# Kernel tuning notes

Hardware: AMD Instinct MI355X
Metric: run time of the kernel (lower is better)

## Reference

```python
import jax, jax.numpy as jnp
import numpy as np

N = 100000   # nodes
E = 600000   # edges
D = 128      # in_dim == out_dim
ED = 6       # edge_dim
LN_EPS = 1e-5


def setup_inputs() -> dict:
    key = jax.random.key(0)
    ks = jax.random.split(key, 12)
    s = 1.0 / np.sqrt(D)
    se = 1.0 / np.sqrt(ED)
    return {
        "x": jax.random.normal(ks[0], (N, D), dtype=jnp.float32),
        "edge_index": jax.random.randint(ks[1], (2, E), 0, N, dtype=jnp.int64),
        "edge_attr": jax.random.normal(ks[2], (E, ED), dtype=jnp.float32),
        "batch": jnp.zeros((N,), dtype=jnp.int64),
        "W_e": jax.random.uniform(ks[3], (ED, D), jnp.float32, -se, se),
        "b_e": jax.random.uniform(ks[4], (D,), jnp.float32, -se, se),
        "eps": jnp.zeros((), dtype=jnp.float32),  # GINE train_eps init 0
        "W1": jax.random.uniform(ks[5], (D, D), jnp.float32, -s, s),
        "b1": jax.random.uniform(ks[6], (D,), jnp.float32, -s, s),
        "W2": jax.random.uniform(ks[7], (D, D), jnp.float32, -s, s),
        "b2": jax.random.uniform(ks[8], (D,), jnp.float32, -s, s),
        "gamma": jnp.ones((D,), dtype=jnp.float32),
        "beta": jnp.zeros((D,), dtype=jnp.float32),
    }


def reference(x, edge_index, edge_attr, batch, W_e, b_e, eps, W1, b1, W2, b2, gamma, beta):
    src, dst = edge_index[0], edge_index[1]
    # edge embedding: Linear(edge_dim -> in_dim)
    edge_emb = edge_attr @ W_e + b_e                      # [E, D]
    # GINEConv message: ReLU(x_j + edge_emb), scatter-add to target nodes
    msg = jax.nn.relu(x[src] + edge_emb)                  # [E, D]
    agg = jax.ops.segment_sum(msg, dst, num_segments=N)   # [N, D]
    h = (1.0 + eps) * x + agg                             # [N, D]
    # GINE nn: Linear -> ReLU -> Linear
    h = jax.nn.relu(h @ W1 + b1) @ W2 + b2                # [N, D]
    # LayerNorm over feature dim
    mu = jnp.mean(h, axis=-1, keepdims=True)
    var = jnp.var(h, axis=-1, keepdims=True)
    h = (h - mu) * jax.lax.rsqrt(var + LN_EPS) * gamma + beta
    # activation=True -> ReLU; dropout identity in eval mode
    return jax.nn.relu(h)
```

## Files before the change

### kernel.cpp

```cpp
#include <hip/hip_runtime.h>
#include <stdint.h>

#define NN 100000
#define EE 600000
#define DD 128

typedef _Float16 half8 __attribute__((ext_vector_type(8)));
typedef _Float16 h2 __attribute__((ext_vector_type(2)));
typedef float f32x4 __attribute__((ext_vector_type(4)));

static __device__ __forceinline__ uint32_t pack2(float a, float b) {
    h2 h; h.x = (_Float16)a; h.y = (_Float16)b;
    return __builtin_bit_cast(uint32_t, h);
}
static __device__ __forceinline__ h2 cvt22(float2 f) {
    h2 r; r.x = (_Float16)f.x; r.y = (_Float16)f.y; return r;
}
static __device__ __forceinline__ h2 bc_lo(h2 v) { h2 r; r.x = v.x; r.y = v.x; return r; }
static __device__ __forceinline__ h2 bc_hi(h2 v) { h2 r; r.x = v.y; r.y = v.y; return r; }

static __device__ __forceinline__ uint32_t edge_msg2(uint32_t rY, uint32_t rZ, uint32_t rW,
                                                     uint32_t xv, uint32_t bb,
                                                     uint32_t w0, uint32_t w1, uint32_t w2,
                                                     uint32_t w3, uint32_t w4, uint32_t w5)
{
    uint32_t m;
    asm("v_pk_fma_f16 %0, %1, %2, %3 op_sel:[0,0,0] op_sel_hi:[0,1,1]"
        : "=v"(m) : "v"(rY), "v"(w0), "v"(bb));
    asm("v_pk_fma_f16 %0, %1, %2, %0 op_sel:[1,0,0] op_sel_hi:[1,1,1]" : "+v"(m) : "v"(rY), "v"(w1));
    asm("v_pk_fma_f16 %0, %1, %2, %0 op_sel:[0,0,0] op_sel_hi:[0,1,1]" : "+v"(m) : "v"(rZ), "v"(w2));
    asm("v_pk_fma_f16 %0, %1, %2, %0 op_sel:[1,0,0] op_sel_hi:[1,1,1]" : "+v"(m) : "v"(rZ), "v"(w3));
    asm("v_pk_fma_f16 %0, %1, %2, %0 op_sel:[0,0,0] op_sel_hi:[0,1,1]" : "+v"(m) : "v"(rW), "v"(w4));
    asm("v_pk_fma_f16 %0, %1, %2, %0 op_sel:[1,0,0] op_sel_hi:[1,1,1]" : "+v"(m) : "v"(rW), "v"(w5));
    asm("v_pk_add_f16 %0, %0, %1" : "+v"(m) : "v"(xv));
    asm("v_pk_max_f16 %0, %0, 0" : "+v"(m));
    return m;
}

#define NB_HIST ((EE + 255) / 256)
#define NB_CONV (NN * DD / 4 / 256)
template<bool CONV>
__global__ __launch_bounds__(256)
void setup_kernel(const int* __restrict__ ei, const float* __restrict__ x,
                  const float* __restrict__ W1, const float* __restrict__ W2,
                  int* __restrict__ counts, uint32_t* __restrict__ xh,
                  _Float16* __restrict__ w1h, _Float16* __restrict__ w2h)
{
    const int nbc = CONV ? NB_CONV : 0;
    const int b = blockIdx.x, tid = threadIdx.x;
    if (b < NB_HIST) {
        int e = b * 256 + tid;
        if (e < EE) atomicAdd(&counts[ei[EE + e]], 1);
    } else if (CONV && b < NB_HIST + nbc) {
        int i = (b - NB_HIST) * 256 + tid;
        float4 v = ((const float4*)x)[i];
        uint2 o; o.x = pack2(v.x, v.y); o.y = pack2(v.z, v.w);
        ((uint2*)xh)[i] = o;
    } else {
        int t = (b - NB_HIST - nbc) * 256 + tid;
        if (t < 2 * DD * DD) {
            int which = t >> 14;
            int idx = t & (DD * DD - 1);
            int k = idx >> 7, d = idx & 127;
            float wv = (which ? W2 : W1)[k * DD + d];
            int kt = k >> 5, kr = k & 31;
            int grp = kr >> 3, j = kr & 7;
            int nt = d >> 4, cc = d & 15;
            int off = ((kt * 8 + nt) * 64 + grp * 16 + cc) * 8 + j;
            (which ? w2h : w1h)[off] = (_Float16)wv;
        }
    }
}

__global__ __launch_bounds__(256)
void scan_blocks(const int* __restrict__ counts, int* __restrict__ startv,
                 int* __restrict__ bsum)
{
    const int t = threadIdx.x;
    const int idx = blockIdx.x * 1024 + t * 4;
    int4 v = {0, 0, 0, 0};
    if (idx < NN) v = *(const int4*)(counts + idx);
    int s1 = v.x + v.y, s2 = s1 + v.z, s3 = s2 + v.w;
    const int lane = t & 63;
    int q = s3;
#pragma unroll
    for (int off = 1; off < 64; off <<= 1) {
        int u = __shfl_up(q, off, 64);
        if (lane >= off) q += u;
    }
    __shared__ int wsum[4];
    if (lane == 63) wsum[t >> 6] = q;
    __syncthreads();
    const int w = t >> 6;
    int pre = 0;
    if (w > 0) pre += wsum[0];
    if (w > 1) pre += wsum[1];
    if (w > 2) pre += wsum[2];
    const int excl = (q - s3) + pre;
    if (idx < NN) {
        int4 o = {excl, excl + v.x, excl + s1, excl + s2};
        *(int4*)(startv + idx) = o;
    }
    __syncthreads();
    if (t == 0) bsum[blockIdx.x] = wsum[0] + wsum[1] + wsum[2] + wsum[3];
}

__global__ __launch_bounds__(128)
void scan_top(const int* __restrict__ bsum, int* __restrict__ boff)
{
    __shared__ int sm[128];
    const int t = threadIdx.x;
    const int NB = (NN + 1023) / 1024;
    int v = (t < NB) ? bsum[t] : 0;
    sm[t] = v;
    __syncthreads();
#pragma unroll
    for (int off = 1; off < 128; off <<= 1) {
        int u = (t >= off) ? sm[t - off] : 0;
        __syncthreads();
        sm[t] += u;
        __syncthreads();
    }
    boff[t] = sm[t] - v;
}

__global__ __launch_bounds__(256)
void scatter_rec(const int* __restrict__ ei, const float* __restrict__ ea,
                 const int* __restrict__ start, const int* __restrict__ boff,
                 int* __restrict__ cursor, float* __restrict__ rec)
{
    int e = blockIdx.x * 256 + threadIdx.x;
    if (e >= EE) return;
    int dst = ei[EE + e];
    int src = ei[e];
    int pos = start[dst] + boff[dst >> 10] + atomicAdd(&cursor[dst], 1);
    const float2* eap = (const float2*)(ea + e * 6);
    float2 e01 = eap[0];
    float2 e23 = eap[1];
    float2 e45 = eap[2];
    float4 r;
    r.x = __int_as_float(src << 6);
    r.y = __uint_as_float(pack2(e01.x, e01.y));
    r.z = __uint_as_float(pack2(e23.x, e23.y));
    r.w = __uint_as_float(pack2(e45.x, e45.y));
    *(float4*)(rec + (size_t)pos * 4) = r;
}

#define NWAVE 8192
__global__ __launch_bounds__(256)
void agg_stream(const uint32_t* __restrict__ xh,
                const float4* __restrict__ rec, const float* __restrict__ We,
                const float* __restrict__ be, const int* __restrict__ start,
                const int* __restrict__ boff, const float* __restrict__ epsp,
                uint32_t* __restrict__ h0h)
{
    const int w = blockIdx.x * 4 + (threadIdx.x >> 6);
    const int lane = threadIdx.x & 63;
    const int d0 = lane * 2;
    const uint32_t w0u = __builtin_bit_cast(uint32_t, cvt22(*(const float2*)(We + 0 * DD + d0)));
    const uint32_t w1u = __builtin_bit_cast(uint32_t, cvt22(*(const float2*)(We + 1 * DD + d0)));
    const uint32_t w2u = __builtin_bit_cast(uint32_t, cvt22(*(const float2*)(We + 2 * DD + d0)));
    const uint32_t w3u = __builtin_bit_cast(uint32_t, cvt22(*(const float2*)(We + 3 * DD + d0)));
    const uint32_t w4u = __builtin_bit_cast(uint32_t, cvt22(*(const float2*)(We + 4 * DD + d0)));
    const uint32_t w5u = __builtin_bit_cast(uint32_t, cvt22(*(const float2*)(We + 5 * DD + d0)));
    const uint32_t bbu = __builtin_bit_cast(uint32_t, cvt22(*(const float2*)(be + d0)));
    const float sc = 1.0f + epsp[0];
    const int n0 = (int)(((long long)w * NN) >> 13);
    const int n1 = (int)(((long long)(w + 1) * NN) >> 13);
    const int span = n1 - n0;

    int gs = 0;
    {
        int nidx = n0 + lane;
        if (lane <= span) {
            gs = (nidx < NN) ? (start[nidx] + boff[nidx >> 10]) : EE;
        }
    }
    const int ebase = __shfl(gs, 0, 64);
    const int eend  = __shfl(gs, span, 64);

    int n = n0;
    int nstop = __shfl(gs, 1, 64);
    h2 xnh = __builtin_bit_cast(h2, xh[((uint32_t)n0 << 6) + lane]);
    float ax = 0.f, ay = 0.f;

#define STEP(K, MK)                                                              \
    {                                                                            \
        const int ek = e + K;                                                    \
        if (ek < eend) {                                                         \
            while (ek >= nstop) {                                                \
                h0h[(size_t)n * 64 + lane] =                                     \
                    pack2(fmaf(sc, (float)xnh.x, ax), fmaf(sc, (float)xnh.y, ay)); \
                ax = 0.f; ay = 0.f; ++n;                                         \
                xnh = __builtin_bit_cast(h2, xh[((uint32_t)n << 6) + lane]);     \
                nstop = __shfl(gs, n - n0 + 1, 64);                              \
            }                                                                    \
            h2 mh = __builtin_bit_cast(h2, MK);                                  \
            ax += (float)mh.x; ay += (float)mh.y;                                \
        }                                                                        \
    }

    for (int e = ebase; e < eend; e += 8) {
        const int last = eend - 1;
        int idx[8];
        float4 r[8];
        uint32_t xv[8], m[8];
#pragma unroll
        for (int k = 0; k < 8; ++k) {
            int ik = e + k;
            idx[k] = ik < eend ? ik : last;
        }
#pragma unroll
        for (int k = 0; k < 8; ++k) r[k] = rec[idx[k]];
#pragma unroll
        for (int k = 0; k < 8; ++k)
            xv[k] = xh[(uint32_t)__float_as_int(r[k].x) + lane];
#pragma unroll
        for (int k = 0; k < 8; ++k)
            m[k] = edge_msg2(__float_as_uint(r[k].y), __float_as_uint(r[k].z),
                             __float_as_uint(r[k].w), xv[k], bbu,
                             w0u, w1u, w2u, w3u, w4u, w5u);
        STEP(0, m[0])
        STEP(1, m[1])
        STEP(2, m[2])
        STEP(3, m[3])
        STEP(4, m[4])
        STEP(5, m[5])
        STEP(6, m[6])
        STEP(7, m[7])
    }
#undef STEP

    while (n < n1) {
        h0h[(size_t)n * 64 + lane] = pack2(fmaf(sc, (float)xnh.x, ax), fmaf(sc, (float)xnh.y, ay));
        ax = 0.f; ay = 0.f; ++n;
        if (n < n1) xnh = __builtin_bit_cast(h2, xh[((uint32_t)n << 6) + lane]);
    }
}

__global__ __launch_bounds__(256)
void agg_pk(const float* __restrict__ x, const float* __restrict__ rec,
            const float* __restrict__ We, const float* __restrict__ be,
            const int* __restrict__ start, const int* __restrict__ boff,
            const int* __restrict__ counts, const float* __restrict__ epsp,
            uint32_t* __restrict__ h0h)
{
    const int w = blockIdx.x * 4 + (threadIdx.x >> 6);
    const int lane = threadIdx.x & 63;
    const int d0 = lane * 2;
    const h2 w0h = cvt22(*(const float2*)(We + 0 * DD + d0));
    const h2 w1h = cvt22(*(const float2*)(We + 1 * DD + d0));
    const h2 w2h = cvt22(*(const float2*)(We + 2 * DD + d0));
    const h2 w3h = cvt22(*(const float2*)(We + 3 * DD + d0));
    const h2 w4h = cvt22(*(const float2*)(We + 4 * DD + d0));
    const h2 w5h = cvt22(*(const float2*)(We + 5 * DD + d0));
    const h2 bbh = cvt22(*(const float2*)(be + d0));
    h2 zero2; zero2.x = (_Float16)0.f; zero2.y = (_Float16)0.f;
    const float sc = 1.0f + epsp[0];
    const int n0 = (int)(((long long)w * NN) >> 13);
    const int n1 = (int)(((long long)(w + 1) * NN) >> 13);

    for (int n = n0; n < n1; ++n) {
        const int begin = start[n] + boff[n >> 10];
        const int cnt = counts[n];
        const float4* rp = (const float4*)rec + begin;
        float ax = 0.f, ay = 0.f;
        for (int i = 0; i < cnt; ++i) {
            float4 r = rp[i];
            int s64 = __float_as_int(r.x);
            h2 c01 = __builtin_bit_cast(h2, r.y);
            h2 c23 = __builtin_bit_cast(h2, r.z);
            h2 c45 = __builtin_bit_cast(h2, r.w);
            h2 emb = bbh;
            emb = bc_lo(c01) * w0h + emb;
            emb = bc_hi(c01) * w1h + emb;
            emb = bc_lo(c23) * w2h + emb;
            emb = bc_hi(c23) * w3h + emb;
            emb = bc_lo(c45) * w4h + emb;
            emb = bc_hi(c45) * w5h + emb;
            h2 m = emb + cvt22(*(const float2*)(x + (size_t)s64 * 2 + d0));
            m = __builtin_elementwise_max(m, zero2);
            ax += (float)m.x;
            ay += (float)m.y;
        }
        float2 xn = *(const float2*)(x + (size_t)n * DD + d0);
        h0h[(size_t)n * 64 + lane] = pack2(fmaf(sc, xn.x, ax), fmaf(sc, xn.y, ay));
    }
}

__global__ __launch_bounds__(256)
void prep_w(const float* __restrict__ W1, const float* __restrict__ W2,
            _Float16* __restrict__ w1h, _Float16* __restrict__ w2h)
{
    int t = blockIdx.x * 256 + threadIdx.x;
    if (t >= 2 * DD * DD) return;
    int which = t >> 14;
    int idx = t & (DD * DD - 1);
    int k = idx >> 7, d = idx & 127;
    float wv = (which ? W2 : W1)[k * DD + d];
    int kt = k >> 5, kr = k & 31;
    int grp = kr >> 3, j = kr & 7;
    int nt = d >> 4, cc = d & 15;
    int off = ((kt * 8 + nt) * 64 + grp * 16 + cc) * 8 + j;
    (which ? w2h : w1h)[off] = (_Float16)wv;
}

__global__ __launch_bounds__(256)
void edge_kernel(const float* __restrict__ x, const int* __restrict__ ei,
                 const float* __restrict__ ea, const float* __restrict__ We,
                 const float* __restrict__ be, float* agg)
{
    int tid = blockIdx.x * 256 + threadIdx.x;
    int d0 = (tid & 31) * 4;
    float4 w0 = *(const float4*)(We + 0 * DD + d0);
    float4 w1 = *(const float4*)(We + 1 * DD + d0);
    float4 w2 = *(const float4*)(We + 2 * DD + d0);
    float4 w3 = *(const float4*)(We + 3 * DD + d0);
    float4 w4 = *(const float4*)(We + 4 * DD + d0);
    float4 w5 = *(const float4*)(We + 5 * DD + d0);
    float4 bb = *(const float4*)(be + d0);
    int estride = (gridDim.x * 256) >> 5;
    for (int e = tid >> 5; e < EE; e += estride) {
        int src = ei[e];
        int dst = ei[EE + e];
        const float2* eap = (const float2*)(ea + e * 6);
        float2 e01 = eap[0];
        float2 e23 = eap[1];
        float2 e45 = eap[2];
        float4 xj = *(const float4*)(x + (size_t)src * DD + d0);
        float mx = xj.x + bb.x + e01.x*w0.x + e01.y*w1.x + e23.x*w2.x + e23.y*w3.x + e45.x*w4.x + e45.y*w5.x;
        float my = xj.y + bb.y + e01.x*w0.y + e01.y*w1.y + e23.x*w2.y + e23.y*w3.y + e45.x*w4.y + e45.y*w5.y;
        float mz = xj.z + bb.z + e01.x*w0.z + e01.y*w1.z + e23.x*w2.z + e23.y*w3.z + e45.x*w4.z + e45.y*w5.z;
        float mw = xj.w + bb.w + e01.x*w0.w + e01.y*w1.w + e23.x*w2.w + e23.y*w3.w + e45.x*w4.w + e45.y*w5.w;
        float* ap = agg + (size_t)dst * DD + d0;
        atomicAdd(ap + 0, fmaxf(mx, 0.f));
        atomicAdd(ap + 1, fmaxf(my, 0.f));
        atomicAdd(ap + 2, fmaxf(mz, 0.f));
        atomicAdd(ap + 3, fmaxf(mw, 0.f));
    }
}

__global__ __launch_bounds__(256)
void node_f16(const uint32_t* __restrict__ h0h,
              const _Float16* __restrict__ w1h, const _Float16* __restrict__ w2h,
              const float* __restrict__ b1, const float* __restrict__ b2,
              const float* __restrict__ gamma, const float* __restrict__ beta,
              float* __restrict__ out)
{
    __shared__ _Float16 h1buf[4][16 * 128];
    const int wv = threadIdx.x >> 6;
    const int l  = threadIdx.x & 63;
    const int lm = l & 15;
    const int lg = l >> 4;
    const int rbase = blockIdx.x * 128 + wv * 32;

    float gam[8], bet[8];
#pragma unroll
    for (int nt = 0; nt < 8; ++nt) {
        gam[nt] = gamma[nt * 16 + lm];
        bet[nt] = beta[nt * 16 + lm];
    }

    for (int t = 0; t < 2; ++t) {
        const int r0 = rbase + t * 16;
        int arow = r0 + lm;
        if (arow >= NN) arow = NN - 1;

        half8 a1[4];
#pragma unroll
        for (int kt = 0; kt < 4; ++kt) {
            const int kb = kt * 32 + lg * 8;
            a1[kt] = *(const half8*)((const _Float16*)h0h + (size_t)arow * DD + kb);
        }

        f32x4 acc[8];
#pragma unroll
        for (int nt = 0; nt < 8; ++nt) { acc[nt][0]=0.f; acc[nt][1]=0.f; acc[nt][2]=0.f; acc[nt][3]=0.f; }
#pragma unroll
        for (int kt = 0; kt < 4; ++kt) {
#pragma unroll
            for (int nt = 0; nt < 8; ++nt) {
                half8 bh = *(const half8*)(w1h + ((size_t)((kt * 8 + nt) * 64 + l)) * 8);
                acc[nt] = __builtin_amdgcn_mfma_f32_16x16x32_f16(a1[kt], bh, acc[nt], 0, 0, 0);
            }
        }

        _Float16* hb = h1buf[wv];
#pragma unroll
        for (int nt = 0; nt < 8; ++nt) {
            const int col = nt * 16 + lm;
            const float bias = b1[col];
#pragma unroll
            for (int q = 0; q < 4; ++q) {
                const int row = lg * 4 + q;
                float v1 = fmaxf(acc[nt][q] + bias, 0.f);
                hb[row * 128 + (col ^ ((row & 7) << 4))] = (_Float16)v1;
            }
        }

        half8 a2[4];
        {
            const int sw = (lm & 7) << 4;
            const _Float16* rowp = hb + lm * 128;
#pragma unroll
            for (int kt = 0; kt < 4; ++kt) {
                const int kb = kt * 32 + lg * 8;
                a2[kt] = *(const half8*)(rowp + (kb ^ sw));
            }
        }

        f32x4 acc2[8];
#pragma unroll
        for (int nt = 0; nt < 8; ++nt) { acc2[nt][0]=0.f; acc2[nt][1]=0.f; acc2[nt][2]=0.f; acc2[nt][3]=0.f; }
#pragma unroll
        for (int kt = 0; kt < 4; ++kt) {
#pragma unroll
            for (int nt = 0; nt < 8; ++nt) {
                half8 bh = *(const half8*)(w2h + ((size_t)((kt * 8 + nt) * 64 + l)) * 8);
                acc2[nt] = __builtin_amdgcn_mfma_f32_16x16x32_f16(a2[kt], bh, acc2[nt], 0, 0, 0);
            }
        }

        float vv[8][4];
        float sums[4] = {0,0,0,0}, sqs[4] = {0,0,0,0};
#pragma unroll
        for (int nt = 0; nt < 8; ++nt) {
            const int col = nt * 16 + lm;
            const float bias = b2[col];
#pragma unroll
            for (int q = 0; q < 4; ++q) {
                float v2 = acc2[nt][q] + bias;
                vv[nt][q] = v2;
                sums[q] += v2;
                sqs[q]  += v2 * v2;
            }
        }
#pragma unroll
        for (int m = 1; m < 16; m <<= 1) {
#pragma unroll
            for (int q = 0; q < 4; ++q) {
                sums[q] += __shfl_xor(sums[q], m, 64);
                sqs[q]  += __shfl_xor(sqs[q],  m, 64);
            }
        }
#pragma unroll
        for (int q = 0; q < 4; ++q) {
            const int grow = r0 + lg * 4 + q;
            if (grow < NN) {
                const float mu  = sums[q] * (1.f / 128.f);
                const float var = sqs[q] * (1.f / 128.f) - mu * mu;
                const float rs  = rsqrtf(var + 1e-5f);
#pragma unroll
                for (int nt = 0; nt < 8; ++nt) {
                    out[(size_t)grow * DD + nt * 16 + lm] =
                        fmaxf((vv[nt][q] - mu) * rs * gam[nt] + bet[nt], 0.f);
                }
            }
        }
    }
}

__global__ __launch_bounds__(256)
void node2c(const float* __restrict__ aggp, const float* __restrict__ xp,
            const _Float16* __restrict__ w1h, const _Float16* __restrict__ w2h,
            const float* __restrict__ b1, const float* __restrict__ b2,
            const float* __restrict__ gamma, const float* __restrict__ beta,
            const float* __restrict__ epsp, float* __restrict__ out)
{
    __shared__ _Float16 h1buf[4][16 * 128];
    const int wv = threadIdx.x >> 6;
    const int l  = threadIdx.x & 63;
    const int lm = l & 15;
    const int lg = l >> 4;
    const int rbase = blockIdx.x * 128 + wv * 32;

    float gam[8], bet[8];
#pragma unroll
    for (int nt = 0; nt < 8; ++nt) {
        gam[nt] = gamma[nt * 16 + lm];
        bet[nt] = beta[nt * 16 + lm];
    }

    for (int t = 0; t < 2; ++t) {
        const int r0 = rbase + t * 16;
        int arow = r0 + lm;
        if (arow >= NN) arow = NN - 1;

        half8 a1[4];
#pragma unroll
        for (int kt = 0; kt < 4; ++kt) {
            const int kb = kt * 32 + lg * 8;
            const float4* hp = (const float4*)(aggp + (size_t)arow * DD + kb);
            float4 p0 = hp[0], p1 = hp[1];
            const float scale = 1.0f + epsp[0];
            const float4* xr = (const float4*)(xp + (size_t)arow * DD + kb);
            float4 x0 = xr[0], x1 = xr[1];
            float v[8] = { x0.x*scale+p0.x, x0.y*scale+p0.y, x0.z*scale+p0.z, x0.w*scale+p0.w,
                           x1.x*scale+p1.x, x1.y*scale+p1.y, x1.z*scale+p1.z, x1.w*scale+p1.w };
#pragma unroll
            for (int j = 0; j < 8; ++j) a1[kt][j] = (_Float16)v[j];
        }

        f32x4 acc[8];
#pragma unroll
        for (int nt = 0; nt < 8; ++nt) { acc[nt][0]=0.f; acc[nt][1]=0.f; acc[nt][2]=0.f; acc[nt][3]=0.f; }
#pragma unroll
        for (int kt = 0; kt < 4; ++kt) {
#pragma unroll
            for (int nt = 0; nt < 8; ++nt) {
                half8 bh = *(const half8*)(w1h + ((size_t)((kt * 8 + nt) * 64 + l)) * 8);
                acc[nt] = __builtin_amdgcn_mfma_f32_16x16x32_f16(a1[kt], bh, acc[nt], 0, 0, 0);
            }
        }

        _Float16* hb = h1buf[wv];
#pragma unroll
        for (int nt = 0; nt < 8; ++nt) {
            const int col = nt * 16 + lm;
            const float bias = b1[col];
#pragma unroll
            for (int q = 0; q < 4; ++q) {
                const int row = lg * 4 + q;
                float v1 = fmaxf(acc[nt][q] + bias, 0.f);
                hb[row * 128 + (col ^ ((row & 7) << 4))] = (_Float16)v1;
            }
        }

        half8 a2[4];
        {
            const int sw = (lm & 7) << 4;
            const _Float16* rowp = hb + lm * 128;
#pragma unroll
            for (int kt = 0; kt < 4; ++kt) {
                const int kb = kt * 32 + lg * 8;
                a2[kt] = *(const half8*)(rowp + (kb ^ sw));
            }
        }

        f32x4 acc2[8];
#pragma unroll
        for (int nt = 0; nt < 8; ++nt) { acc2[nt][0]=0.f; acc2[nt][1]=0.f; acc2[nt][2]=0.f; acc2[nt][3]=0.f; }
#pragma unroll
        for (int kt = 0; kt < 4; ++kt) {
#pragma unroll
            for (int nt = 0; nt < 8; ++nt) {
                half8 bh = *(const half8*)(w2h + ((size_t)((kt * 8 + nt) * 64 + l)) * 8);
                acc2[nt] = __builtin_amdgcn_mfma_f32_16x16x32_f16(a2[kt], bh, acc2[nt], 0, 0, 0);
            }
        }

        float vv[8][4];
        float sums[4] = {0,0,0,0}, sqs[4] = {0,0,0,0};
#pragma unroll
        for (int nt = 0; nt < 8; ++nt) {
            const int col = nt * 16 + lm;
            const float bias = b2[col];
#pragma unroll
            for (int q = 0; q < 4; ++q) {
                float v2 = acc2[nt][q] + bias;
                vv[nt][q] = v2;
                sums[q] += v2;
                sqs[q]  += v2 * v2;
            }
        }
#pragma unroll
        for (int m = 1; m < 16; m <<= 1) {
#pragma unroll
            for (int q = 0; q < 4; ++q) {
                sums[q] += __shfl_xor(sums[q], m, 64);
                sqs[q]  += __shfl_xor(sqs[q],  m, 64);
            }
        }
#pragma unroll
        for (int q = 0; q < 4; ++q) {
            const int grow = r0 + lg * 4 + q;
            if (grow < NN) {
                const float mu  = sums[q] * (1.f / 128.f);
                const float var = sqs[q] * (1.f / 128.f) - mu * mu;
                const float rs  = rsqrtf(var + 1e-5f);
#pragma unroll
                for (int nt = 0; nt < 8; ++nt) {
                    out[(size_t)grow * DD + nt * 16 + lm] =
                        fmaxf((vv[nt][q] - mu) * rs * gam[nt] + bet[nt], 0.f);
                }
            }
        }
    }
}

extern "C" void kernel_launch(void* const* d_in, const int* in_sizes, int n_in,
                              void* d_out, int out_size, void* d_ws, size_t ws_size,
                              hipStream_t stream) {
    (void)in_sizes; (void)n_in; (void)out_size;
    const float* x     = (const float*)d_in[0];
    const int*   ei    = (const int*)d_in[1];
    const float* ea    = (const float*)d_in[2];
    const float* We    = (const float*)d_in[4];
    const float* be    = (const float*)d_in[5];
    const float* epsp  = (const float*)d_in[6];
    const float* W1    = (const float*)d_in[7];
    const float* b1    = (const float*)d_in[8];
    const float* W2    = (const float*)d_in[9];
    const float* b2    = (const float*)d_in[10];
    const float* gamma = (const float*)d_in[11];
    const float* beta  = (const float*)d_in[12];
    float* out = (float*)d_out;

    char* ws = (char*)d_ws;
    _Float16* w1h = (_Float16*)ws;
    _Float16* w2h = w1h + DD * DD;
    size_t off = 2 * (size_t)DD * DD * sizeof(_Float16);
    int* counts = (int*)(ws + off);   off += (size_t)NN * 4;
    int* cursor = (int*)(ws + off);   off += (size_t)NN * 4;
    int* start  = (int*)(ws + off);   off += (size_t)NN * 4;
    int* bsum   = (int*)(ws + off);   off += 512;
    int* boff   = (int*)(ws + off);   off += 512;
    float* rec  = (float*)(ws + off); off += (size_t)EE * 16;
    uint32_t* h0h = (uint32_t*)(ws + off); off += (size_t)NN * DD * 2;
    const size_t need_h0 = off;
    uint32_t* xh  = (uint32_t*)(ws + off); off += (size_t)NN * DD * 2;
    const size_t need_xh = off;

    const int node_blocks = (NN + 127) / 128;
    const int NBLK = (NN + 1023) / 1024;

    if (ws_size >= need_h0) {
        const bool conv = (ws_size >= need_xh);
        hipMemsetAsync(counts, 0, 2 * (size_t)NN * 4, stream);
        if (conv) {
            setup_kernel<true><<<NB_HIST + NB_CONV + 128, 256, 0, stream>>>(
                ei, x, W1, W2, counts, xh, w1h, w2h);
        } else {
            setup_kernel<false><<<NB_HIST + 128, 256, 0, stream>>>(
                ei, x, W1, W2, counts, xh, w1h, w2h);
        }
        scan_blocks<<<NBLK, 256, 0, stream>>>(counts, start, bsum);
        scan_top<<<1, 128, 0, stream>>>(bsum, boff);
        scatter_rec<<<(EE + 255) / 256, 256, 0, stream>>>(ei, ea, start, boff, cursor, rec);
        if (conv) {
            agg_stream<<<NWAVE / 4, 256, 0, stream>>>(xh, (const float4*)rec, We, be,
                                                      start, boff, epsp, h0h);
        } else {
            agg_pk<<<NWAVE / 4, 256, 0, stream>>>(x, rec, We, be, start, boff,
                                                  counts, epsp, h0h);
        }
        node_f16<<<node_blocks, 256, 0, stream>>>(h0h, w1h, w2h, b1, b2, gamma, beta, out);
    } else {
        hipMemsetAsync(d_out, 0, (size_t)NN * DD * sizeof(float), stream);
        prep_w<<<(2 * DD * DD + 255) / 256, 256, 0, stream>>>(W1, W2, w1h, w2h);
        edge_kernel<<<2048, 256, 0, stream>>>(x, ei, ea, We, be, out);
        node2c<<<node_blocks, 256, 0, stream>>>(out, x, w1h, w2h, b1, b2,
                                                gamma, beta, epsp, out);
    }
}
```

Measured before the change: 160.5 us.

## Fuse edge aggregation with node MLP and LayerNorm in one kernel

```diff
diff --git a/kernel.cpp b/kernel.cpp
--- a/kernel.cpp
+++ b/kernel.cpp
@@ -146,98 +146,218 @@
     *(float4*)(rec + (size_t)pos * 4) = r;
 }
 
+__global__ __launch_bounds__(256)
+void fused_an(const uint32_t* __restrict__ xh, const float4* __restrict__ rec,
+              const float* __restrict__ We, const float* __restrict__ be,
+              const int* __restrict__ start, const int* __restrict__ boff,
+              const float* __restrict__ epsp,
+              const _Float16* __restrict__ w1h, const _Float16* __restrict__ w2h,
+              const float* __restrict__ b1, const float* __restrict__ b2,
+              const float* __restrict__ gamma, const float* __restrict__ beta,
+              float* __restrict__ out)
+{
+    __shared__ _Float16 hbuf[4][16 * 128];
+    const int wv = threadIdx.x >> 6;
+    const int lane = threadIdx.x & 63;
+    const int n0w = blockIdx.x * 64 + wv * 16;
+    _Float16* hb = hbuf[wv];
+
+    if (n0w < NN) {
+        int n1w = n0w + 16; if (n1w > NN) n1w = NN;
+        const int span = n1w - n0w;
+        const int d0 = lane * 2;
+        const uint32_t w0u = __builtin_bit_cast(uint32_t, cvt22(*(const float2*)(We + 0 * DD + d0)));
+        const uint32_t w1u = __builtin_bit_cast(uint32_t, cvt22(*(const float2*)(We + 1 * DD + d0)));
+        const uint32_t w2u = __builtin_bit_cast(uint32_t, cvt22(*(const float2*)(We + 2 * DD + d0)));
+        const uint32_t w3u = __builtin_bit_cast(uint32_t, cvt22(*(const float2*)(We + 3 * DD + d0)));
+        const uint32_t w4u = __builtin_bit_cast(uint32_t, cvt22(*(const float2*)(We + 4 * DD + d0)));
+        const uint32_t w5u = __builtin_bit_cast(uint32_t, cvt22(*(const float2*)(We + 5 * DD + d0)));
+        const uint32_t bbu = __builtin_bit_cast(uint32_t, cvt22(*(const float2*)(be + d0)));
+        const float sc = 1.0f + epsp[0];
+
+        int gs = 0;
+        {
+            int nidx = n0w + lane;
+            if (lane <= span) gs = (nidx < NN) ? (start[nidx] + boff[nidx >> 10]) : EE;
+        }
+        const int ebase = __shfl(gs, 0, 64);
+        const int eend  = __shfl(gs, span, 64);
+
+        int n = n0w;
+        int nstop = __shfl(gs, 1, 64);
+        h2 xnh = __builtin_bit_cast(h2, xh[((uint32_t)n0w << 6) + lane]);
+        float ax = 0.f, ay = 0.f;
+
+#define FLUSH_H0()                                                               \
+        {                                                                        \
+            const int row = n - n0w;                                             \
+            *(uint32_t*)&hb[row * 128 + (d0 ^ ((row & 7) << 4))] =               \
+                pack2(fmaf(sc, (float)xnh.x, ax), fmaf(sc, (float)xnh.y, ay));   \
+        }
+
+#define STEP(K, MK)                                                              \
+        {                                                                        \
+            const int ek = e + K;                                                \
+            if (ek < eend) {                                                     \
+                while (ek >= nstop) {                                            \
+                    FLUSH_H0();                                                  \
+                    ax = 0.f; ay = 0.f; ++n;                                     \
+                    xnh = __builtin_bit_cast(h2, xh[((uint32_t)n << 6) + lane]); \
+                    nstop = __shfl(gs, n - n0w + 1, 64);                         \
+                }                                                                \
+                h2 mh = __builtin_bit_cast(h2, MK);                              \
+                ax += (float)mh.x; ay += (float)mh.y;                            \
+            }                                                                    \
+        }
+
+        for (int e = ebase; e < eend; e += 8) {
+            const int last = eend - 1;
+            int idx[8];
+            float4 r[8];
+            uint32_t xv[8], m[8];
+#pragma unroll
+            for (int k = 0; k < 8; ++k) {
+                int ik = e + k;
+                idx[k] = ik < eend ? ik : last;
+            }
+#pragma unroll
+            for (int k = 0; k < 8; ++k) r[k] = rec[idx[k]];
+#pragma unroll
+            for (int k = 0; k < 8; ++k)
+                xv[k] = xh[(uint32_t)__float_as_int(r[k].x) + lane];
+#pragma unroll
+            for (int k = 0; k < 8; ++k)
+                m[k] = edge_msg2(__float_as_uint(r[k].y), __float_as_uint(r[k].z),
+                                 __float_as_uint(r[k].w), xv[k], bbu,
+                                 w0u, w1u, w2u, w3u, w4u, w5u);
+            STEP(0, m[0])
+            STEP(1, m[1])
+            STEP(2, m[2])
+            STEP(3, m[3])
+            STEP(4, m[4])
+            STEP(5, m[5])
+            STEP(6, m[6])
+            STEP(7, m[7])
+        }
+#undef STEP
+
+        while (n < n1w) {
+            FLUSH_H0();
+            ax = 0.f; ay = 0.f; ++n;
+            if (n < n1w) xnh = __builtin_bit_cast(h2, xh[((uint32_t)n << 6) + lane]);
+        }
+#undef FLUSH_H0
+    }
+
+    const int l  = lane;
+    const int lm = l & 15;
+    const int lg = l >> 4;
+    const int r0 = n0w;
+
+    float gam[8], bet[8];
+#pragma unroll
+    for (int nt = 0; nt < 8; ++nt) {
+        gam[nt] = gamma[nt * 16 + lm];
+        bet[nt] = beta[nt * 16 + lm];
+    }
+
+    half8 a1[4];
+    {
+        const int sw = (lm & 7) << 4;
+        const _Float16* rowp = hb + lm * 128;
+#pragma unroll
+        for (int kt = 0; kt < 4; ++kt) {
+            const int kb = kt * 32 + lg * 8;
+            a1[kt] = *(const half8*)(rowp + (kb ^ sw));
+        }
+    }
+
+    f32x4 acc[8];
+#pragma unroll
+    for (int nt = 0; nt < 8; ++nt) { acc[nt][0]=0.f; acc[nt][1]=0.f; acc[nt][2]=0.f; acc[nt][3]=0.f; }
+#pragma unroll
+    for (int kt = 0; kt < 4; ++kt) {
+#pragma unroll
+        for (int nt = 0; nt < 8; ++nt) {
+            half8 bh = *(const half8*)(w1h + ((size_t)((kt * 8 + nt) * 64 + l)) * 8);
+            acc[nt] = __builtin_amdgcn_mfma_f32_16x16x32_f16(a1[kt], bh, acc[nt], 0, 0, 0);
+        }
+    }
+
+#pragma unroll
+    for (int nt = 0; nt < 8; ++nt) {
+        const int col = nt * 16 + lm;
+        const float bias = b1[col];
+#pragma unroll
+        for (int q = 0; q < 4; ++q) {
+            const int row = lg * 4 + q;
+            float v1 = fmaxf(acc[nt][q] + bias, 0.f);
+            hb[row * 128 + (col ^ ((row & 7) << 4))] = (_Float16)v1;
+        }
+    }
+
+    half8 a2[4];
+    {
+        const int sw = (lm & 7) << 4;
+        const _Float16* rowp = hb + lm * 128;
+#pragma unroll
+        for (int kt = 0; kt < 4; ++kt) {
+            const int kb = kt * 32 + lg * 8;
+            a2[kt] = *(const half8*)(rowp + (kb ^ sw));
+        }
+    }
+
+    f32x4 acc2[8];
+#pragma unroll
+    for (int nt = 0; nt < 8; ++nt) { acc2[nt][0]=0.f; acc2[nt][1]=0.f; acc2[nt][2]=0.f; acc2[nt][3]=0.f; }
+#pragma unroll
+    for (int kt = 0; kt < 4; ++kt) {
+#pragma unroll
+        for (int nt = 0; nt < 8; ++nt) {
+            half8 bh = *(const half8*)(w2h + ((size_t)((kt * 8 + nt) * 64 + l)) * 8);
+            acc2[nt] = __builtin_amdgcn_mfma_f32_16x16x32_f16(a2[kt], bh, acc2[nt], 0, 0, 0);
+        }
+    }
+
+    float vv[8][4];
+    float sums[4] = {0,0,0,0}, sqs[4] = {0,0,0,0};
+#pragma unroll
+    for (int nt = 0; nt < 8; ++nt) {
+        const int col = nt * 16 + lm;
+        const float bias = b2[col];
+#pragma unroll
+        for (int q = 0; q < 4; ++q) {
+            float v2 = acc2[nt][q] + bias;
+            vv[nt][q] = v2;
+            sums[q] += v2;
+            sqs[q]  += v2 * v2;
+        }
+    }
+#pragma unroll
+    for (int m = 1; m < 16; m <<= 1) {
+#pragma unroll
+        for (int q = 0; q < 4; ++q) {
+            sums[q] += __shfl_xor(sums[q], m, 64);
+            sqs[q]  += __shfl_xor(sqs[q],  m, 64);
+        }
+    }
+#pragma unroll
+    for (int q = 0; q < 4; ++q) {
+        const int grow = r0 + lg * 4 + q;
+        if (grow < NN) {
+            const float mu  = sums[q] * (1.f / 128.f);
+            const float var = sqs[q] * (1.f / 128.f) - mu * mu;
+            const float rs  = rsqrtf(var + 1e-5f);
+#pragma unroll
+            for (int nt = 0; nt < 8; ++nt) {
+                out[(size_t)grow * DD + nt * 16 + lm] =
+                    fmaxf((vv[nt][q] - mu) * rs * gam[nt] + bet[nt], 0.f);
+            }
+        }
+    }
+}
+
 #define NWAVE 8192
-__global__ __launch_bounds__(256)
-void agg_stream(const uint32_t* __restrict__ xh,
-                const float4* __restrict__ rec, const float* __restrict__ We,
-                const float* __restrict__ be, const int* __restrict__ start,
-                const int* __restrict__ boff, const float* __restrict__ epsp,
-                uint32_t* __restrict__ h0h)
-{
-    const int w = blockIdx.x * 4 + (threadIdx.x >> 6);
-    const int lane = threadIdx.x & 63;
-    const int d0 = lane * 2;
-    const uint32_t w0u = __builtin_bit_cast(uint32_t, cvt22(*(const float2*)(We + 0 * DD + d0)));
-    const uint32_t w1u = __builtin_bit_cast(uint32_t, cvt22(*(const float2*)(We + 1 * DD + d0)));
-    const uint32_t w2u = __builtin_bit_cast(uint32_t, cvt22(*(const float2*)(We + 2 * DD + d0)));
-    const uint32_t w3u = __builtin_bit_cast(uint32_t, cvt22(*(const float2*)(We + 3 * DD + d0)));
-    const uint32_t w4u = __builtin_bit_cast(uint32_t, cvt22(*(const float2*)(We + 4 * DD + d0)));
-    const uint32_t w5u = __builtin_bit_cast(uint32_t, cvt22(*(const float2*)(We + 5 * DD + d0)));
-    const uint32_t bbu = __builtin_bit_cast(uint32_t, cvt22(*(const float2*)(be + d0)));
-    const float sc = 1.0f + epsp[0];
-    const int n0 = (int)(((long long)w * NN) >> 13);
-    const int n1 = (int)(((long long)(w + 1) * NN) >> 13);
-    const int span = n1 - n0;
-
-    int gs = 0;
-    {
-        int nidx = n0 + lane;
-        if (lane <= span) {
-            gs = (nidx < NN) ? (start[nidx] + boff[nidx >> 10]) : EE;
-        }
-    }
-    const int ebase = __shfl(gs, 0, 64);
-    const int eend  = __shfl(gs, span, 64);
-
-    int n = n0;
-    int nstop = __shfl(gs, 1, 64);
-    h2 xnh = __builtin_bit_cast(h2, xh[((uint32_t)n0 << 6) + lane]);
-    float ax = 0.f, ay = 0.f;
-
-#define STEP(K, MK)                                                              \
-    {                                                                            \
-        const int ek = e + K;                                                    \
-        if (ek < eend) {                                                         \
-            while (ek >= nstop) {                                                \
-                h0h[(size_t)n * 64 + lane] =                                     \
-                    pack2(fmaf(sc, (float)xnh.x, ax), fmaf(sc, (float)xnh.y, ay)); \
-                ax = 0.f; ay = 0.f; ++n;                                         \
-                xnh = __builtin_bit_cast(h2, xh[((uint32_t)n << 6) + lane]);     \
-                nstop = __shfl(gs, n - n0 + 1, 64);                              \
-            }                                                                    \
-            h2 mh = __builtin_bit_cast(h2, MK);                                  \
-            ax += (float)mh.x; ay += (float)mh.y;                                \
-        }                                                                        \
-    }
-
-    for (int e = ebase; e < eend; e += 8) {
-        const int last = eend - 1;
-        int idx[8];
-        float4 r[8];
-        uint32_t xv[8], m[8];
-#pragma unroll
-        for (int k = 0; k < 8; ++k) {
-            int ik = e + k;
-            idx[k] = ik < eend ? ik : last;
-        }
-#pragma unroll
-        for (int k = 0; k < 8; ++k) r[k] = rec[idx[k]];
-#pragma unroll
-        for (int k = 0; k < 8; ++k)
-            xv[k] = xh[(uint32_t)__float_as_int(r[k].x) + lane];
-#pragma unroll
-        for (int k = 0; k < 8; ++k)
-            m[k] = edge_msg2(__float_as_uint(r[k].y), __float_as_uint(r[k].z),
-                             __float_as_uint(r[k].w), xv[k], bbu,
-                             w0u, w1u, w2u, w3u, w4u, w5u);
-        STEP(0, m[0])
-        STEP(1, m[1])
-        STEP(2, m[2])
-        STEP(3, m[3])
-        STEP(4, m[4])
-        STEP(5, m[5])
-        STEP(6, m[6])
-        STEP(7, m[7])
-    }
-#undef STEP
-
-    while (n < n1) {
-        h0h[(size_t)n * 64 + lane] = pack2(fmaf(sc, (float)xnh.x, ax), fmaf(sc, (float)xnh.y, ay));
-        ax = 0.f; ay = 0.f; ++n;
-        if (n < n1) xnh = __builtin_bit_cast(h2, xh[((uint32_t)n << 6) + lane]);
-    }
-}
-
 __global__ __launch_bounds__(256)
 void agg_pk(const float* __restrict__ x, const float* __restrict__ rec,
             const float* __restrict__ We, const float* __restrict__ be,
@@ -285,6 +405,126 @@
         }
         float2 xn = *(const float2*)(x + (size_t)n * DD + d0);
         h0h[(size_t)n * 64 + lane] = pack2(fmaf(sc, xn.x, ax), fmaf(sc, xn.y, ay));
+    }
+}
+
+__global__ __launch_bounds__(256)
+void node_f16(const uint32_t* __restrict__ h0h,
+              const _Float16* __restrict__ w1h, const _Float16* __restrict__ w2h,
+              const float* __restrict__ b1, const float* __restrict__ b2,
+              const float* __restrict__ gamma, const float* __restrict__ beta,
+              float* __restrict__ out)
+{
+    __shared__ _Float16 h1buf[4][16 * 128];
+    const int wv = threadIdx.x >> 6;
+    const int l  = threadIdx.x & 63;
+    const int lm = l & 15;
+    const int lg = l >> 4;
+    const int rbase = blockIdx.x * 128 + wv * 32;
+
+    float gam[8], bet[8];
+#pragma unroll
+    for (int nt = 0; nt < 8; ++nt) {
+        gam[nt] = gamma[nt * 16 + lm];
+        bet[nt] = beta[nt * 16 + lm];
+    }
+
+    for (int t = 0; t < 2; ++t) {
+        const int r0 = rbase + t * 16;
+        int arow = r0 + lm;
+        if (arow >= NN) arow = NN - 1;
+
+        half8 a1[4];
+#pragma unroll
+        for (int kt = 0; kt < 4; ++kt) {
+            const int kb = kt * 32 + lg * 8;
+            a1[kt] = *(const half8*)((const _Float16*)h0h + (size_t)arow * DD + kb);
+        }
+
+        f32x4 acc[8];
+#pragma unroll
+        for (int nt = 0; nt < 8; ++nt) { acc[nt][0]=0.f; acc[nt][1]=0.f; acc[nt][2]=0.f; acc[nt][3]=0.f; }
+#pragma unroll
+        for (int kt = 0; kt < 4; ++kt) {
+#pragma unroll
+            for (int nt = 0; nt < 8; ++nt) {
+                half8 bh = *(const half8*)(w1h + ((size_t)((kt * 8 + nt) * 64 + l)) * 8);
+                acc[nt] = __builtin_amdgcn_mfma_f32_16x16x32_f16(a1[kt], bh, acc[nt], 0, 0, 0);
+            }
+        }
+
+        _Float16* hb = h1buf[wv];
+#pragma unroll
+        for (int nt = 0; nt < 8; ++nt) {
+            const int col = nt * 16 + lm;
+            const float bias = b1[col];
+#pragma unroll
+            for (int q = 0; q < 4; ++q) {
+                const int row = lg * 4 + q;
+                float v1 = fmaxf(acc[nt][q] + bias, 0.f);
+                hb[row * 128 + (col ^ ((row & 7) << 4))] = (_Float16)v1;
+            }
+        }
+
+        half8 a2[4];
+        {
+            const int sw = (lm & 7) << 4;
+            const _Float16* rowp = hb + lm * 128;
+#pragma unroll
+            for (int kt = 0; kt < 4; ++kt) {
+                const int kb = kt * 32 + lg * 8;
+                a2[kt] = *(const half8*)(rowp + (kb ^ sw));
+            }
+        }
+
+        f32x4 acc2[8];
+#pragma unroll
+        for (int nt = 0; nt < 8; ++nt) { acc2[nt][0]=0.f; acc2[nt][1]=0.f; acc2[nt][2]=0.f; acc2[nt][3]=0.f; }
+#pragma unroll
+        for (int kt = 0; kt < 4; ++kt) {
+#pragma unroll
+            for (int nt = 0; nt < 8; ++nt) {
+                half8 bh = *(const half8*)(w2h + ((size_t)((kt * 8 + nt) * 64 + l)) * 8);
+                acc2[nt] = __builtin_amdgcn_mfma_f32_16x16x32_f16(a2[kt], bh, acc2[nt], 0, 0, 0);
+            }
+        }
+
+        float vv[8][4];
+        float sums[4] = {0,0,0,0}, sqs[4] = {0,0,0,0};
+#pragma unroll
+        for (int nt = 0; nt < 8; ++nt) {
+            const int col = nt * 16 + lm;
+            const float bias = b2[col];
+#pragma unroll
+            for (int q = 0; q < 4; ++q) {
+                float v2 = acc2[nt][q] + bias;
+                vv[nt][q] = v2;
+                sums[q] += v2;
+                sqs[q]  += v2 * v2;
+            }
+        }
+#pragma unroll
+        for (int m = 1; m < 16; m <<= 1) {
+#pragma unroll
+            for (int q = 0; q < 4; ++q) {
+                sums[q] += __shfl_xor(sums[q], m, 64);
+                sqs[q]  += __shfl_xor(sqs[q],  m, 64);
+            }
+        }
+#pragma unroll
+        for (int q = 0; q < 4; ++q) {
+            const int grow = r0 + lg * 4 + q;
+            if (grow < NN) {
+                const float mu  = sums[q] * (1.f / 128.f);
+                const float var = sqs[q] * (1.f / 128.f) - mu * mu;
+                const float rs  = rsqrtf(var + 1e-5f);
+#pragma unroll
+                for (int nt = 0; nt < 8; ++nt) {
+                    out[(size_t)grow * DD + nt * 16 + lm] =
+                        fmaxf((vv[nt][q] - mu) * rs * gam[nt] + bet[nt], 0.f);
+                }
+            }
+        }
     }
 }
 
@@ -341,126 +581,6 @@
 }
 
 __global__ __launch_bounds__(256)
-void node_f16(const uint32_t* __restrict__ h0h,
-              const _Float16* __restrict__ w1h, const _Float16* __restrict__ w2h,
-              const float* __restrict__ b1, const float* __restrict__ b2,
-              const float* __restrict__ gamma, const float* __restrict__ beta,
-              float* __restrict__ out)
-{
-    __shared__ _Float16 h1buf[4][16 * 128];
-    const int wv = threadIdx.x >> 6;
-    const int l  = threadIdx.x & 63;
-    const int lm = l & 15;
-    const int lg = l >> 4;
-    const int rbase = blockIdx.x * 128 + wv * 32;
-
-    float gam[8], bet[8];
-#pragma unroll
-    for (int nt = 0; nt < 8; ++nt) {
-        gam[nt] = gamma[nt * 16 + lm];
-        bet[nt] = beta[nt * 16 + lm];
-    }
-
-    for (int t = 0; t < 2; ++t) {
-        const int r0 = rbase + t * 16;
-        int arow = r0 + lm;
-        if (arow >= NN) arow = NN - 1;
-
-        half8 a1[4];
-#pragma unroll
-        for (int kt = 0; kt < 4; ++kt) {
-            const int kb = kt * 32 + lg * 8;
-            a1[kt] = *(const half8*)((const _Float16*)h0h + (size_t)arow * DD + kb);
-        }
-
-        f32x4 acc[8];
-#pragma unroll
-        for (int nt = 0; nt < 8; ++nt) { acc[nt][0]=0.f; acc[nt][1]=0.f; acc[nt][2]=0.f; acc[nt][3]=0.f; }
-#pragma unroll
-        for (int kt = 0; kt < 4; ++kt) {
-#pragma unroll
-            for (int nt = 0; nt < 8; ++nt) {
-                half8 bh = *(const half8*)(w1h + ((size_t)((kt * 8 + nt) * 64 + l)) * 8);
-                acc[nt] = __builtin_amdgcn_mfma_f32_16x16x32_f16(a1[kt], bh, acc[nt], 0, 0, 0);
-            }
-        }
-
-        _Float16* hb = h1buf[wv];
-#pragma unroll
-        for (int nt = 0; nt < 8; ++nt) {
-            const int col = nt * 16 + lm;
-            const float bias = b1[col];
-#pragma unroll
-            for (int q = 0; q < 4; ++q) {
-                const int row = lg * 4 + q;
-                float v1 = fmaxf(acc[nt][q] + bias, 0.f);
-                hb[row * 128 + (col ^ ((row & 7) << 4))] = (_Float16)v1;
-            }
-        }
-
-        half8 a2[4];
-        {
-            const int sw = (lm & 7) << 4;
-            const _Float16* rowp = hb + lm * 128;
-#pragma unroll
-            for (int kt = 0; kt < 4; ++kt) {
-                const int kb = kt * 32 + lg * 8;
-                a2[kt] = *(const half8*)(rowp + (kb ^ sw));
-            }
-        }
-
-        f32x4 acc2[8];
-#pragma unroll
-        for (int nt = 0; nt < 8; ++nt) { acc2[nt][0]=0.f; acc2[nt][1]=0.f; acc2[nt][2]=0.f; acc2[nt][3]=0.f; }
-#pragma unroll
-        for (int kt = 0; kt < 4; ++kt) {
-#pragma unroll
-            for (int nt = 0; nt < 8; ++nt) {
-                half8 bh = *(const half8*)(w2h + ((size_t)((kt * 8 + nt) * 64 + l)) * 8);
-                acc2[nt] = __builtin_amdgcn_mfma_f32_16x16x32_f16(a2[kt], bh, acc2[nt], 0, 0, 0);
-            }
-        }
-
-        float vv[8][4];
-        float sums[4] = {0,0,0,0}, sqs[4] = {0,0,0,0};
-#pragma unroll
-        for (int nt = 0; nt < 8; ++nt) {
-            const int col = nt * 16 + lm;
-            const float bias = b2[col];
-#pragma unroll
-            for (int q = 0; q < 4; ++q) {
-                float v2 = acc2[nt][q] + bias;
-                vv[nt][q] = v2;
-                sums[q] += v2;
-                sqs[q]  += v2 * v2;
-            }
-        }
-#pragma unroll
-        for (int m = 1; m < 16; m <<= 1) {
-#pragma unroll
-            for (int q = 0; q < 4; ++q) {
-                sums[q] += __shfl_xor(sums[q], m, 64);
-                sqs[q]  += __shfl_xor(sqs[q],  m, 64);
-            }
-        }
-#pragma unroll
-        for (int q = 0; q < 4; ++q) {
-            const int grow = r0 + lg * 4 + q;
-            if (grow < NN) {
-                const float mu  = sums[q] * (1.f / 128.f);
-                const float var = sqs[q] * (1.f / 128.f) - mu * mu;
-                const float rs  = rsqrtf(var + 1e-5f);
-#pragma unroll
-                for (int nt = 0; nt < 8; ++nt) {
-                    out[(size_t)grow * DD + nt * 16 + lm] =
-                        fmaxf((vv[nt][q] - mu) * rs * gam[nt] + bet[nt], 0.f);
-                }
-            }
-        }
-    }
-}
-
-__global__ __launch_bounds__(256)
 void node2c(const float* __restrict__ aggp, const float* __restrict__ xp,
             const _Float16* __restrict__ w1h, const _Float16* __restrict__ w2h,
             const float* __restrict__ b1, const float* __restrict__ b2,
@@ -622,6 +742,7 @@
     const size_t need_xh = off;
 
     const int node_blocks = (NN + 127) / 128;
+    const int fused_blocks = (NN + 63) / 64;
     const int NBLK = (NN + 1023) / 1024;
 
     if (ws_size >= need_h0) {
@@ -638,13 +759,14 @@
         scan_top<<<1, 128, 0, stream>>>(bsum, boff);
         scatter_rec<<<(EE + 255) / 256, 256, 0, stream>>>(ei, ea, start, boff, cursor, rec);
         if (conv) {
-            agg_stream<<<NWAVE / 4, 256, 0, stream>>>(xh, (const float4*)rec, We, be,
-                                                      start, boff, epsp, h0h);
+            fused_an<<<fused_blocks, 256, 0, stream>>>(xh, (const float4*)rec, We, be,
+                                                       start, boff, epsp, w1h, w2h,
+                                                       b1, b2, gamma, beta, out);
         } else {
             agg_pk<<<NWAVE / 4, 256, 0, stream>>>(x, rec, We, be, start, boff,
                                                   counts, epsp, h0h);
-        }
-        node_f16<<<node_blocks, 256, 0, stream>>>(h0h, w1h, w2h, b1, b2, gamma, beta, out);
+            node_f16<<<node_blocks, 256, 0, stream>>>(h0h, w1h, w2h, b1, b2, gamma, beta, out);
+        }
     } else {
         hipMemsetAsync(d_out, 0, (size_t)NN * DD * sizeof(float), stream);
         prep_w<<<(2 * DD * DD + 255) / 256, 256, 0, stream>>>(W1, W2, w1h, w2h);
```

After: 156.2 us. -2.7%, faster.
